# Kernel tuning notes

Measured on AMD Instinct MI355X. Metric: run time of the kernel, lower is better.

Reference implementation:

```python
import jax, jax.numpy as jnp
import numpy as np

N_POINTS = 8192
N_TOPICS = 64
B = 524288


def setup_inputs() -> dict:
    key = jax.random.key(0)
    k1, k2, k3, k4 = jax.random.split(key, 4)
    pij = jax.random.uniform(k1, (B,), dtype=jnp.float32, minval=1e-6, maxval=1.0)
    i = jax.random.randint(k2, (B,), 0, N_POINTS, dtype=jnp.int64)
    j = jax.random.randint(k3, (B,), 0, N_POINTS, dtype=jnp.int64)
    W = jax.random.normal(k4, (N_POINTS, N_TOPICS), dtype=jnp.float32)  # nn.Embedding weight
    return {"pij": pij, "i": i, "j": j, "W": W}


def reference(pij, i, j, W):
    # pairwise squared distances over ALL points, via the gram trick
    # (avoids materializing the [n, n, d] broadcasted tensor of the torch code)
    sq = jnp.sum(W * W, axis=1)                       # [n]
    d2 = sq[:, None] + sq[None, :] - 2.0 * (W @ W.T)  # [n, n]
    d2 = jnp.maximum(d2, 0.0)                         # numerical floor (exact math is >= 0)
    n = W.shape[0]
    # Cauchy kernel partition: sum_{k,l} 1/(1+d2) minus the n diagonal ones
    part = jnp.sum(1.0 / (1.0 + d2)) - jnp.asarray(n, d2.dtype)
    xi = W[i]                                         # [B, d]
    xj = W[j]                                         # [B, d]
    # FAITHFUL to source: (1 + diff^2).sum(1) adds 1 per dim => n_topics + ||xi-xj||^2
    num = 1.0 / jnp.sum(1.0 + (xi - xj) ** 2, axis=1)  # [B]
    qij = num / part
    loss_kld = pij * (jnp.log(pij) - jnp.log(qij))
    return jnp.sum(loss_kld)
```

## Files before the change

kernel.cpp:

```cpp
#include <hip/hip_runtime.h>
#include <math.h>

#define NPOINTS   8192
#define NDIM      64
#define TILE      128
#define NT2       64
#define NBLK      2080
#define NPAIR_BLK 2048

#define WS_W16   0
#define WS_SQ    262144
#define WS_PARTA 270336
#define WS_A1P   272416
#define WS_A3P   274464

typedef __attribute__((ext_vector_type(8))) short bf16x8;
typedef __attribute__((ext_vector_type(4))) float f32x4;

__device__ inline unsigned short f2bf(float f) {
    unsigned u = __float_as_uint(f);
    u += 0x7FFFu + ((u >> 16) & 1u);
    return (unsigned short)(u >> 16);
}
__device__ inline float bflo(unsigned u) { return __uint_as_float(u << 16); }
__device__ inline float bfhi(unsigned u) { return __uint_as_float(u & 0xFFFF0000u); }

__global__ __launch_bounds__(256) void prep_kernel(const float* __restrict__ W,
                                                   float* __restrict__ sq,
                                                   unsigned* __restrict__ W16) {
    int wid  = (blockIdx.x * 256 + threadIdx.x) >> 6;
    int lane = threadIdx.x & 63;
    float v = W[wid * NDIM + lane];
    float s = v * v;
    #pragma unroll
    for (int m = 32; m >= 1; m >>= 1) s += __shfl_xor(s, m, 64);
    if (lane == 0) sq[wid] = s;
    unsigned bf   = f2bf(v);
    unsigned peer = (unsigned)__shfl_xor((int)bf, 1, 64);
    if ((lane & 1) == 0)
        W16[wid * 32 + (lane >> 1)] = (bf & 0xFFFFu) | (peer << 16);
}

__global__ __launch_bounds__(256) void pairwise_kernel(const unsigned* __restrict__ W16,
                                                       const float* __restrict__ sq,
                                                       float* __restrict__ partA) {
    int z = blockIdx.x;
    int by = (int)((129.0 - sqrt(16641.0 - 8.0 * (double)z)) * 0.5);
    while (by * NT2 - by * (by - 1) / 2 > z) --by;
    while ((by + 1) * NT2 - (by + 1) * by / 2 <= z) ++by;
    int bx = by + (z - (by * NT2 - by * (by - 1) / 2));

    int t = threadIdx.x, w = t >> 6, lane = t & 63;
    int wm = w >> 1, wn = w & 1, quad = lane >> 4, l15 = lane & 15;
    int a0 = by * TILE, b0 = bx * TILE;

    float base1[4][4], sqb[4];
    {
        int arow = a0 + wm * 64 + quad * 4;
        #pragma unroll
        for (int tm = 0; tm < 4; ++tm)
            #pragma unroll
            for (int r = 0; r < 4; ++r) base1[tm][r] = 1.0f + sq[arow + tm * 16 + r];
        int bcol = b0 + wn * 64 + l15;
        #pragma unroll
        for (int tn = 0; tn < 4; ++tn) sqb[tn] = sq[bcol + tn * 16];
    }

    f32x4 acc[4][4];
    #pragma unroll
    for (int i = 0; i < 4; ++i)
        #pragma unroll
        for (int j = 0; j < 4; ++j) acc[i][j] = (f32x4){0.f, 0.f, 0.f, 0.f};

    const unsigned* Arow = W16 + (a0 + wm * 64 + l15) * 32;
    const unsigned* Brow = W16 + (b0 + wn * 64 + l15) * 32;
    #pragma unroll
    for (int h = 0; h < 2; ++h) {
        bf16x8 af[4], bfr[4];
        #pragma unroll
        for (int tm = 0; tm < 4; ++tm)
            af[tm] = *(const bf16x8*)(Arow + tm * 16 * 32 + h * 16 + quad * 4);
        #pragma unroll
        for (int tn = 0; tn < 4; ++tn)
            bfr[tn] = *(const bf16x8*)(Brow + tn * 16 * 32 + h * 16 + quad * 4);
        #pragma unroll
        for (int tm = 0; tm < 4; ++tm)
            #pragma unroll
            for (int tn = 0; tn < 4; ++tn)
                acc[tm][tn] = __builtin_amdgcn_mfma_f32_16x16x32_bf16(af[tm], bfr[tn],
                                                                      acc[tm][tn], 0, 0, 0);
    }

    float ssum = 0.f;
    if (bx > by) {
        #pragma unroll
        for (int tn = 0; tn < 4; ++tn)
            #pragma unroll
            for (int tm = 0; tm < 4; ++tm)
                #pragma unroll
                for (int r = 0; r < 4; ++r) {
                    float c = base1[tm][r] + sqb[tn];
                    ssum += __builtin_amdgcn_rcpf(fmaf(acc[tm][tn][r], -2.0f, c));
                }
    } else {
        #pragma unroll
        for (int tn = 0; tn < 4; ++tn) {
            int cl = wn * 64 + tn * 16 + l15;
            #pragma unroll
            for (int tm = 0; tm < 4; ++tm)
                #pragma unroll
                for (int r = 0; r < 4; ++r) {
                    int rl = wm * 64 + tm * 16 + quad * 4 + r;
                    float c = base1[tm][r] + sqb[tn];
                    float inv = __builtin_amdgcn_rcpf(fmaf(acc[tm][tn][r], -2.0f, c));
                    ssum += (cl > rl) ? inv : 0.f;
                }
        }
    }
    #pragma unroll
    for (int m = 32; m >= 1; m >>= 1) ssum += __shfl_xor(ssum, m, 64);
    __shared__ float wsum[4];
    if (lane == 0) wsum[w] = ssum;
    __syncthreads();
    if (t == 0) partA[z] = wsum[0] + wsum[1] + wsum[2] + wsum[3];
}

__global__ __launch_bounds__(256) void pair_kernel(const unsigned* __restrict__ W16,
                                                   const float* __restrict__ pij,
                                                   const int* __restrict__ ii,
                                                   const int* __restrict__ jj,
                                                   int nb,
                                                   float* __restrict__ a1p,
                                                   float* __restrict__ a3p) {
    int t = threadIdx.x, lane = t & 63;
    int g = lane >> 3;
    int s = lane & 7;
    int wid = (blockIdx.x * 256 + t) >> 6;
    const int nwave = NPAIR_BLK * 4;
    __shared__ float s1[4], s3[4];

    float a1 = 0.f, a3 = 0.f;
    for (int p0 = wid * 16; p0 < nb; p0 += nwave * 16) {
        int  pA = p0 + g,          pB = p0 + 8 + g;
        bool okA = pA < nb,        okB = pB < nb;
        int  cA = okA ? pA : 0,    cB = okB ? pB : 0;
        int   iA = ii[cA], jA = jj[cA];
        int   iB = ii[cB], jB = jj[cB];
        float pvA = pij[cA], pvB = pij[cB];
        uint4 xiA = *(const uint4*)(W16 + iA * 32 + s * 4);
        uint4 xjA = *(const uint4*)(W16 + jA * 32 + s * 4);
        uint4 xiB = *(const uint4*)(W16 + iB * 32 + s * 4);
        uint4 xjB = *(const uint4*)(W16 + jB * 32 + s * 4);

        float vA, vB;
        {
            float d0 = bflo(xiA.x) - bflo(xjA.x), d1 = bfhi(xiA.x) - bfhi(xjA.x);
            float d2 = bflo(xiA.y) - bflo(xjA.y), d3 = bfhi(xiA.y) - bfhi(xjA.y);
            float d4 = bflo(xiA.z) - bflo(xjA.z), d5 = bfhi(xiA.z) - bfhi(xjA.z);
            float d6 = bflo(xiA.w) - bflo(xjA.w), d7 = bfhi(xiA.w) - bfhi(xjA.w);
            vA = d0 * d0;
            vA = fmaf(d1, d1, vA); vA = fmaf(d2, d2, vA); vA = fmaf(d3, d3, vA);
            vA = fmaf(d4, d4, vA); vA = fmaf(d5, d5, vA); vA = fmaf(d6, d6, vA);
            vA = fmaf(d7, d7, vA);
        }
        {
            float d0 = bflo(xiB.x) - bflo(xjB.x), d1 = bfhi(xiB.x) - bfhi(xjB.x);
            float d2 = bflo(xiB.y) - bflo(xjB.y), d3 = bfhi(xiB.y) - bfhi(xjB.y);
            float d4 = bflo(xiB.z) - bflo(xjB.z), d5 = bfhi(xiB.z) - bfhi(xjB.z);
            float d6 = bflo(xiB.w) - bflo(xjB.w), d7 = bfhi(xiB.w) - bfhi(xjB.w);
            vB = d0 * d0;
            vB = fmaf(d1, d1, vB); vB = fmaf(d2, d2, vB); vB = fmaf(d3, d3, vB);
            vB = fmaf(d4, d4, vB); vB = fmaf(d5, d5, vB); vB = fmaf(d7, d7, fmaf(d6, d6, vB));
        }
        #pragma unroll
        for (int m = 1; m <= 4; m <<= 1) {
            vA += __shfl_xor(vA, m, 64);
            vB += __shfl_xor(vB, m, 64);
        }
        float tA = pvA * __logf(pvA * ((float)NDIM + vA));
        float tB = pvB * __logf(pvB * ((float)NDIM + vB));
        a1 += okA ? tA : 0.f;  a3 += okA ? pvA : 0.f;
        a1 += okB ? tB : 0.f;  a3 += okB ? pvB : 0.f;
    }
    #pragma unroll
    for (int m = 32; m >= 1; m >>= 1) {
        a1 += __shfl_xor(a1, m, 64);
        a3 += __shfl_xor(a3, m, 64);
    }
    if (lane == 0) { s1[t >> 6] = a1 * 0.125f; s3[t >> 6] = a3 * 0.125f; }
    __syncthreads();
    if (t == 0) {
        a1p[blockIdx.x] = s1[0] + s1[1] + s1[2] + s1[3];
        a3p[blockIdx.x] = s3[0] + s3[1] + s3[2] + s3[3];
    }
}

__global__ __launch_bounds__(256) void final_kernel(const float* __restrict__ partA,
                                                    const float* __restrict__ a1p,
                                                    const float* __restrict__ a3p,
                                                    float* __restrict__ out) {
    __shared__ double r1[256], r2[256], r3[256];
    int t = threadIdx.x;
    double dpart = 0.0, d1 = 0.0, d3 = 0.0;
    for (int k = t; k < NBLK; k += 256) dpart += (double)partA[k];
    for (int k = t; k < NPAIR_BLK; k += 256) { d1 += (double)a1p[k]; d3 += (double)a3p[k]; }
    r1[t] = dpart; r2[t] = d1; r3[t] = d3;
    __syncthreads();
    for (int s = 128; s >= 1; s >>= 1) {
        if (t < s) { r1[t] += r1[t + s]; r2[t] += r2[t + s]; r3[t] += r3[t + s]; }
        __syncthreads();
    }
    if (t == 0) {
        double part = 2.0 * r1[0];
        out[0] = (float)(r2[0] + r3[0] * log(part));
    }
}

extern "C" void kernel_launch(void* const* d_in, const int* in_sizes, int n_in,
                              void* d_out, int out_size, void* d_ws, size_t ws_size,
                              hipStream_t stream) {
    const float* pij = (const float*)d_in[0];
    const int*   ii  = (const int*)d_in[1];
    const int*   jj  = (const int*)d_in[2];
    const float* W   = (const float*)d_in[3];
    float* out = (float*)d_out;
    float* ws  = (float*)d_ws;

    unsigned* W16  = (unsigned*)ws + WS_W16;
    float*    sqv  = ws + WS_SQ;
    float*    partA = ws + WS_PARTA;
    float*    a1p  = ws + WS_A1P;
    float*    a3p  = ws + WS_A3P;

    int nb = in_sizes[0];

    prep_kernel<<<NPOINTS / 4, 256, 0, stream>>>(W, sqv, W16);
    pairwise_kernel<<<NBLK, 256, 0, stream>>>(W16, sqv, partA);
    pair_kernel<<<NPAIR_BLK, 256, 0, stream>>>(W16, pij, ii, jj, nb, a1p, a3p);
    final_kernel<<<1, 256, 0, stream>>>(partA, a1p, a3p, out);
}
```

Measured before the change: 103.1 us.

## Fuse pairwise gram and pair-loss kernels into one launch with block-range dispatch

Merges the pairwise partition kernel and the sampled-pair KL kernel into a single launch. The first NBLK blocks do the MFMA tile work and the remaining blocks each handle one 16-pair chunk per wave, replacing the old grid-stride loop. This removes one launch and lets the two independent phases overlap on the GPU. The pair path also switches to a dot-product form using the precomputed squared norms, and the sq loads become float4. The a1p/a3p partial buffers grow to 8192 entries, which makes the final reduction larger.

New measurement: 122.2 us. 1.19x slower.

```diff
diff --git a/kernel.cpp b/kernel.cpp
--- a/kernel.cpp
+++ b/kernel.cpp
@@ -6,13 +6,13 @@
 #define TILE      128
 #define NT2       64
 #define NBLK      2080
-#define NPAIR_BLK 2048
+#define NPAIR_BLK 8192
 
 #define WS_W16   0
 #define WS_SQ    262144
 #define WS_PARTA 270336
 #define WS_A1P   272416
-#define WS_A3P   274464
+#define WS_A3P   280608
 
 typedef __attribute__((ext_vector_type(8))) short bf16x8;
 typedef __attribute__((ext_vector_type(4))) float f32x4;
@@ -41,157 +41,169 @@
         W16[wid * 32 + (lane >> 1)] = (bf & 0xFFFFu) | (peer << 16);
 }
 
-__global__ __launch_bounds__(256) void pairwise_kernel(const unsigned* __restrict__ W16,
-                                                       const float* __restrict__ sq,
-                                                       float* __restrict__ partA) {
+__global__ __launch_bounds__(256) void fused_kernel(const unsigned* __restrict__ W16,
+                                                    const float* __restrict__ sq,
+                                                    const float* __restrict__ pij,
+                                                    const int* __restrict__ ii,
+                                                    const int* __restrict__ jj,
+                                                    int nb,
+                                                    float* __restrict__ partA,
+                                                    float* __restrict__ a1p,
+                                                    float* __restrict__ a3p) {
+    __shared__ float red[8];
     int z = blockIdx.x;
-    int by = (int)((129.0 - sqrt(16641.0 - 8.0 * (double)z)) * 0.5);
-    while (by * NT2 - by * (by - 1) / 2 > z) --by;
-    while ((by + 1) * NT2 - (by + 1) * by / 2 <= z) ++by;
-    int bx = by + (z - (by * NT2 - by * (by - 1) / 2));
-
     int t = threadIdx.x, w = t >> 6, lane = t & 63;
-    int wm = w >> 1, wn = w & 1, quad = lane >> 4, l15 = lane & 15;
-    int a0 = by * TILE, b0 = bx * TILE;
-
-    float base1[4][4], sqb[4];
-    {
-        int arow = a0 + wm * 64 + quad * 4;
-        #pragma unroll
-        for (int tm = 0; tm < 4; ++tm)
-            #pragma unroll
-            for (int r = 0; r < 4; ++r) base1[tm][r] = 1.0f + sq[arow + tm * 16 + r];
-        int bcol = b0 + wn * 64 + l15;
-        #pragma unroll
-        for (int tn = 0; tn < 4; ++tn) sqb[tn] = sq[bcol + tn * 16];
-    }
-
-    f32x4 acc[4][4];
-    #pragma unroll
-    for (int i = 0; i < 4; ++i)
-        #pragma unroll
-        for (int j = 0; j < 4; ++j) acc[i][j] = (f32x4){0.f, 0.f, 0.f, 0.f};
-
-    const unsigned* Arow = W16 + (a0 + wm * 64 + l15) * 32;
-    const unsigned* Brow = W16 + (b0 + wn * 64 + l15) * 32;
-    #pragma unroll
-    for (int h = 0; h < 2; ++h) {
-        bf16x8 af[4], bfr[4];
-        #pragma unroll
-        for (int tm = 0; tm < 4; ++tm)
-            af[tm] = *(const bf16x8*)(Arow + tm * 16 * 32 + h * 16 + quad * 4);
-        #pragma unroll
-        for (int tn = 0; tn < 4; ++tn)
-            bfr[tn] = *(const bf16x8*)(Brow + tn * 16 * 32 + h * 16 + quad * 4);
-        #pragma unroll
-        for (int tm = 0; tm < 4; ++tm)
+
+    if (z < NBLK) {
+        int by = (int)((129.0 - sqrt(16641.0 - 8.0 * (double)z)) * 0.5);
+        while (by * NT2 - by * (by - 1) / 2 > z) --by;
+        while ((by + 1) * NT2 - (by + 1) * by / 2 <= z) ++by;
+        int bx = by + (z - (by * NT2 - by * (by - 1) / 2));
+
+        int wm = w >> 1, wn = w & 1, quad = lane >> 4, l15 = lane & 15;
+        int a0 = by * TILE, b0 = bx * TILE;
+
+        float4 base1[4];
+        float  sqb[4];
+        {
+            int arow = a0 + wm * 64 + quad * 4;
+            #pragma unroll
+            for (int tm = 0; tm < 4; ++tm) {
+                float4 v = *(const float4*)(sq + arow + tm * 16);
+                base1[tm] = (float4){1.0f + v.x, 1.0f + v.y, 1.0f + v.z, 1.0f + v.w};
+            }
+            int bcol = b0 + wn * 64 + l15;
+            #pragma unroll
+            for (int tn = 0; tn < 4; ++tn) sqb[tn] = sq[bcol + tn * 16];
+        }
+
+        f32x4 acc[4][4];
+        #pragma unroll
+        for (int i = 0; i < 4; ++i)
+            #pragma unroll
+            for (int j = 0; j < 4; ++j) acc[i][j] = (f32x4){0.f, 0.f, 0.f, 0.f};
+
+        const unsigned* Arow = W16 + (a0 + wm * 64 + l15) * 32;
+        const unsigned* Brow = W16 + (b0 + wn * 64 + l15) * 32;
+        #pragma unroll
+        for (int h = 0; h < 2; ++h) {
+            bf16x8 af[4], bfr[4];
+            #pragma unroll
+            for (int tm = 0; tm < 4; ++tm)
+                af[tm] = *(const bf16x8*)(Arow + tm * 16 * 32 + h * 16 + quad * 4);
             #pragma unroll
             for (int tn = 0; tn < 4; ++tn)
-                acc[tm][tn] = __builtin_amdgcn_mfma_f32_16x16x32_bf16(af[tm], bfr[tn],
-                                                                      acc[tm][tn], 0, 0, 0);
-    }
-
-    float ssum = 0.f;
-    if (bx > by) {
-        #pragma unroll
-        for (int tn = 0; tn < 4; ++tn)
+                bfr[tn] = *(const bf16x8*)(Brow + tn * 16 * 32 + h * 16 + quad * 4);
             #pragma unroll
             for (int tm = 0; tm < 4; ++tm)
                 #pragma unroll
-                for (int r = 0; r < 4; ++r) {
-                    float c = base1[tm][r] + sqb[tn];
-                    ssum += __builtin_amdgcn_rcpf(fmaf(acc[tm][tn][r], -2.0f, c));
+                for (int tn = 0; tn < 4; ++tn)
+                    acc[tm][tn] = __builtin_amdgcn_mfma_f32_16x16x32_bf16(af[tm], bfr[tn],
+                                                                          acc[tm][tn], 0, 0, 0);
+        }
+
+        float ssum = 0.f;
+        if (bx > by) {
+            #pragma unroll
+            for (int tn = 0; tn < 4; ++tn) {
+                float c0 = sqb[tn];
+                #pragma unroll
+                for (int tm = 0; tm < 4; ++tm) {
+                    ssum += __builtin_amdgcn_rcpf(fmaf(acc[tm][tn][0], -2.0f, base1[tm].x + c0));
+                    ssum += __builtin_amdgcn_rcpf(fmaf(acc[tm][tn][1], -2.0f, base1[tm].y + c0));
+                    ssum += __builtin_amdgcn_rcpf(fmaf(acc[tm][tn][2], -2.0f, base1[tm].z + c0));
+                    ssum += __builtin_amdgcn_rcpf(fmaf(acc[tm][tn][3], -2.0f, base1[tm].w + c0));
                 }
+            }
+        } else {
+            int quad4 = quad * 4;
+            #pragma unroll
+            for (int tn = 0; tn < 4; ++tn) {
+                int cl = wn * 64 + tn * 16 + l15;
+                float c0 = sqb[tn];
+                float b4[4] = {0, 0, 0, 0};
+                #pragma unroll
+                for (int tm = 0; tm < 4; ++tm) {
+                    b4[0] = base1[tm].x; b4[1] = base1[tm].y;
+                    b4[2] = base1[tm].z; b4[3] = base1[tm].w;
+                    #pragma unroll
+                    for (int r = 0; r < 4; ++r) {
+                        int rl = wm * 64 + tm * 16 + quad4 + r;
+                        float inv = __builtin_amdgcn_rcpf(fmaf(acc[tm][tn][r], -2.0f, b4[r] + c0));
+                        ssum += (cl > rl) ? inv : 0.f;
+                    }
+                }
+            }
+        }
+        #pragma unroll
+        for (int m = 32; m >= 1; m >>= 1) ssum += __shfl_xor(ssum, m, 64);
+        if (lane == 0) red[w] = ssum;
+        __syncthreads();
+        if (t == 0) partA[z] = red[0] + red[1] + red[2] + red[3];
     } else {
-        #pragma unroll
-        for (int tn = 0; tn < 4; ++tn) {
-            int cl = wn * 64 + tn * 16 + l15;
-            #pragma unroll
-            for (int tm = 0; tm < 4; ++tm)
-                #pragma unroll
-                for (int r = 0; r < 4; ++r) {
-                    int rl = wm * 64 + tm * 16 + quad * 4 + r;
-                    float c = base1[tm][r] + sqb[tn];
-                    float inv = __builtin_amdgcn_rcpf(fmaf(acc[tm][tn][r], -2.0f, c));
-                    ssum += (cl > rl) ? inv : 0.f;
-                }
-        }
-    }
-    #pragma unroll
-    for (int m = 32; m >= 1; m >>= 1) ssum += __shfl_xor(ssum, m, 64);
-    __shared__ float wsum[4];
-    if (lane == 0) wsum[w] = ssum;
-    __syncthreads();
-    if (t == 0) partA[z] = wsum[0] + wsum[1] + wsum[2] + wsum[3];
-}
-
-__global__ __launch_bounds__(256) void pair_kernel(const unsigned* __restrict__ W16,
-                                                   const float* __restrict__ pij,
-                                                   const int* __restrict__ ii,
-                                                   const int* __restrict__ jj,
-                                                   int nb,
-                                                   float* __restrict__ a1p,
-                                                   float* __restrict__ a3p) {
-    int t = threadIdx.x, lane = t & 63;
-    int g = lane >> 3;
-    int s = lane & 7;
-    int wid = (blockIdx.x * 256 + t) >> 6;
-    const int nwave = NPAIR_BLK * 4;
-    __shared__ float s1[4], s3[4];
-
-    float a1 = 0.f, a3 = 0.f;
-    for (int p0 = wid * 16; p0 < nb; p0 += nwave * 16) {
-        int  pA = p0 + g,          pB = p0 + 8 + g;
-        bool okA = pA < nb,        okB = pB < nb;
-        int  cA = okA ? pA : 0,    cB = okB ? pB : 0;
-        int   iA = ii[cA], jA = jj[cA];
-        int   iB = ii[cB], jB = jj[cB];
-        float pvA = pij[cA], pvB = pij[cB];
-        uint4 xiA = *(const uint4*)(W16 + iA * 32 + s * 4);
-        uint4 xjA = *(const uint4*)(W16 + jA * 32 + s * 4);
-        uint4 xiB = *(const uint4*)(W16 + iB * 32 + s * 4);
-        uint4 xjB = *(const uint4*)(W16 + jB * 32 + s * 4);
-
-        float vA, vB;
-        {
-            float d0 = bflo(xiA.x) - bflo(xjA.x), d1 = bfhi(xiA.x) - bfhi(xjA.x);
-            float d2 = bflo(xiA.y) - bflo(xjA.y), d3 = bfhi(xiA.y) - bfhi(xjA.y);
-            float d4 = bflo(xiA.z) - bflo(xjA.z), d5 = bfhi(xiA.z) - bfhi(xjA.z);
-            float d6 = bflo(xiA.w) - bflo(xjA.w), d7 = bfhi(xiA.w) - bfhi(xjA.w);
-            vA = d0 * d0;
-            vA = fmaf(d1, d1, vA); vA = fmaf(d2, d2, vA); vA = fmaf(d3, d3, vA);
-            vA = fmaf(d4, d4, vA); vA = fmaf(d5, d5, vA); vA = fmaf(d6, d6, vA);
-            vA = fmaf(d7, d7, vA);
-        }
-        {
-            float d0 = bflo(xiB.x) - bflo(xjB.x), d1 = bfhi(xiB.x) - bfhi(xjB.x);
-            float d2 = bflo(xiB.y) - bflo(xjB.y), d3 = bfhi(xiB.y) - bfhi(xjB.y);
-            float d4 = bflo(xiB.z) - bflo(xjB.z), d5 = bfhi(xiB.z) - bfhi(xjB.z);
-            float d6 = bflo(xiB.w) - bflo(xjB.w), d7 = bfhi(xiB.w) - bfhi(xjB.w);
-            vB = d0 * d0;
-            vB = fmaf(d1, d1, vB); vB = fmaf(d2, d2, vB); vB = fmaf(d3, d3, vB);
-            vB = fmaf(d4, d4, vB); vB = fmaf(d5, d5, vB); vB = fmaf(d7, d7, fmaf(d6, d6, vB));
-        }
-        #pragma unroll
-        for (int m = 1; m <= 4; m <<= 1) {
-            vA += __shfl_xor(vA, m, 64);
-            vB += __shfl_xor(vB, m, 64);
-        }
-        float tA = pvA * __logf(pvA * ((float)NDIM + vA));
-        float tB = pvB * __logf(pvB * ((float)NDIM + vB));
-        a1 += okA ? tA : 0.f;  a3 += okA ? pvA : 0.f;
-        a1 += okB ? tB : 0.f;  a3 += okB ? pvB : 0.f;
-    }
-    #pragma unroll
-    for (int m = 32; m >= 1; m >>= 1) {
-        a1 += __shfl_xor(a1, m, 64);
-        a3 += __shfl_xor(a3, m, 64);
-    }
-    if (lane == 0) { s1[t >> 6] = a1 * 0.125f; s3[t >> 6] = a3 * 0.125f; }
-    __syncthreads();
-    if (t == 0) {
-        a1p[blockIdx.x] = s1[0] + s1[1] + s1[2] + s1[3];
-        a3p[blockIdx.x] = s3[0] + s3[1] + s3[2] + s3[3];
+        int pb = z - NBLK;
+        int p0 = (pb * 4 + w) * 16;
+        float a1 = 0.f, a3 = 0.f;
+        if (p0 < nb) {
+            int g = lane >> 3;
+            int s = lane & 7;
+            int  pA = p0 + g,        pB = p0 + 8 + g;
+            bool okA = pA < nb,      okB = pB < nb;
+            int  cA = okA ? pA : 0,  cB = okB ? pB : 0;
+            int   iA = ii[cA], jA = jj[cA];
+            int   iB = ii[cB], jB = jj[cB];
+            float pvA = pij[cA], pvB = pij[cB];
+            uint4 xiA = *(const uint4*)(W16 + iA * 32 + s * 4);
+            uint4 xjA = *(const uint4*)(W16 + jA * 32 + s * 4);
+            uint4 xiB = *(const uint4*)(W16 + iB * 32 + s * 4);
+            uint4 xjB = *(const uint4*)(W16 + jB * 32 + s * 4);
+            float sA = sq[iA] + sq[jA];
+            float sB = sq[iB] + sq[jB];
+
+            float dA, dB;
+            {
+                dA = bflo(xiA.x) * bflo(xjA.x);
+                dA = fmaf(bfhi(xiA.x), bfhi(xjA.x), dA);
+                dA = fmaf(bflo(xiA.y), bflo(xjA.y), dA);
+                dA = fmaf(bfhi(xiA.y), bfhi(xjA.y), dA);
+                dA = fmaf(bflo(xiA.z), bflo(xjA.z), dA);
+                dA = fmaf(bfhi(xiA.z), bfhi(xjA.z), dA);
+                dA = fmaf(bflo(xiA.w), bflo(xjA.w), dA);
+                dA = fmaf(bfhi(xiA.w), bfhi(xjA.w), dA);
+            }
+            {
+                dB = bflo(xiB.x) * bflo(xjB.x);
+                dB = fmaf(bfhi(xiB.x), bfhi(xjB.x), dB);
+                dB = fmaf(bflo(xiB.y), bflo(xjB.y), dB);
+                dB = fmaf(bfhi(xiB.y), bfhi(xjB.y), dB);
+                dB = fmaf(bflo(xiB.z), bflo(xjB.z), dB);
+                dB = fmaf(bfhi(xiB.z), bfhi(xjB.z), dB);
+                dB = fmaf(bflo(xiB.w), bflo(xjB.w), dB);
+                dB = fmaf(bfhi(xiB.w), bfhi(xjB.w), dB);
+            }
+            #pragma unroll
+            for (int m = 1; m <= 4; m <<= 1) {
+                dA += __shfl_xor(dA, m, 64);
+                dB += __shfl_xor(dB, m, 64);
+            }
+            float vA = fmaf(dA, -2.0f, sA);
+            float vB = fmaf(dB, -2.0f, sB);
+            float tA = pvA * __logf(pvA * ((float)NDIM + vA));
+            float tB = pvB * __logf(pvB * ((float)NDIM + vB));
+            a1 += okA ? tA : 0.f;  a3 += okA ? pvA : 0.f;
+            a1 += okB ? tB : 0.f;  a3 += okB ? pvB : 0.f;
+        }
+        #pragma unroll
+        for (int m = 32; m >= 1; m >>= 1) {
+            a1 += __shfl_xor(a1, m, 64);
+            a3 += __shfl_xor(a3, m, 64);
+        }
+        if (lane == 0) { red[w] = a1 * 0.125f; red[4 + w] = a3 * 0.125f; }
+        __syncthreads();
+        if (t == 0) {
+            a1p[pb] = red[0] + red[1] + red[2] + red[3];
+            a3p[pb] = red[4] + red[5] + red[6] + red[7];
+        }
     }
 }
 
@@ -226,16 +238,16 @@
     float* out = (float*)d_out;
     float* ws  = (float*)d_ws;
 
-    unsigned* W16  = (unsigned*)ws + WS_W16;
-    float*    sqv  = ws + WS_SQ;
+    unsigned* W16   = (unsigned*)ws + WS_W16;
+    float*    sqv   = ws + WS_SQ;
     float*    partA = ws + WS_PARTA;
-    float*    a1p  = ws + WS_A1P;
-    float*    a3p  = ws + WS_A3P;
+    float*    a1p   = ws + WS_A1P;
+    float*    a3p   = ws + WS_A3P;
 
     int nb = in_sizes[0];
 
     prep_kernel<<<NPOINTS / 4, 256, 0, stream>>>(W, sqv, W16);
-    pairwise_kernel<<<NBLK, 256, 0, stream>>>(W16, sqv, partA);
-    pair_kernel<<<NPAIR_BLK, 256, 0, stream>>>(W16, pij, ii, jj, nb, a1p, a3p);
+    fused_kernel<<<NBLK + NPAIR_BLK, 256, 0, stream>>>(W16, sqv, pij, ii, jj, nb,
+                                                       partA, a1p, a3p);
     final_kernel<<<1, 256, 0, stream>>>(partA, a1p, a3p, out);
 }
```
